# Kernel tuning notes

Measured on AMD Instinct MI355X. Metric: run time of the kernel, lower is better.

Reference implementation:

```python
import jax, jax.numpy as jnp
import numpy as np

NB = 8      # n_blocks
DIM = 256   # model dim (= context_len in source)
DI = 512    # dim_inner = dim * expand(2)
DCONV = 4   # depthwise conv kernel
NS = 16     # d_state
DTR = 16    # dt_rank = ceil(dim/16)
NE = 4      # experts
INNER = 512 # MoE FFN inner = dim * multi(2)
L = 8192    # sequence length
HOR = 32    # horizon
EPS = 1e-3


def setup_inputs() -> dict:
    key = jax.random.key(0)
    ks = jax.random.split(key, 16)
    s = 0.02
    f = lambda k, shp: jax.random.normal(k, shp, jnp.float32) * s
    return {
        "x": jax.random.normal(ks[0], (DIM, L), jnp.float32),
        "lin_w": f(ks[1], (DIM, DIM)),                      # shared by self.linear and self.out (tied)
        "in_proj_w": f(ks[2], (NB, 2 * DI, DIM)),
        "conv_w": f(ks[3], (NB, DI, 1, DCONV)),             # depthwise conv, groups=DI
        "conv_b": f(ks[4], (NB, DI)),
        "x_proj_w": f(ks[5], (NB, DTR + 2 * NS, DI)),
        "dt_proj_w": f(ks[6], (NB, DI, DTR)),
        "dt_proj_b": f(ks[7], (NB, DI)),
        "A_log": jnp.tile(jnp.log(jnp.arange(1, NS + 1, dtype=jnp.float32)), (NB, DI, 1)),
        "D_param": jnp.ones((NB, DI), jnp.float32),
        "out_proj_w": f(ks[8], (NB, DIM, DI)),
        "gate_w": f(ks[9], (NB, NE, DIM)),
        "gproj_w": f(ks[10], (NB, NE, INNER, DIM)),
        "uproj_w": f(ks[11], (NB, NE, INNER, DIM)),
        "dproj_w": f(ks[12], (NB, NE, DIM, INNER)),
        "rms_a_w": jnp.ones((DIM,), jnp.float32),
        "rms_f_w": jnp.ones((DIM,), jnp.float32),
        "head_w1": f(ks[13], (DIM, DIM)),
        "head_w2": f(ks[14], (HOR, DIM)),
    }


def _rmsnorm(h, w):
    return w * (h * jax.lax.rsqrt(jnp.mean(h * h, axis=-1, keepdims=True) + EPS))


def _mamba(h, ipw, cw, cb, xpw, dtw, dtb, alog, dpar, opw):
    b = h.shape[0]
    xr = jnp.einsum('bld,od->bol', h, ipw)            # (b, 2*DI, l)
    xc, res = jnp.split(xr, 2, axis=1)                # each (b, DI, l)
    # causal depthwise conv (padding=DCONV-1, sliced to length l)
    xc = jax.lax.conv_general_dilated(xc, cw, (1,), [(DCONV - 1, 0)],
                                      feature_group_count=DI,
                                      dimension_numbers=('NCH', 'OIH', 'NCH'))
    xc = jax.nn.silu(xc + cb[None, :, None])
    A = -jnp.exp(alog)                                # (DI, NS)
    xdbl = jnp.einsum('bdl,kd->blk', xc, xpw)         # (b, l, DTR+2*NS)
    dr, B, C = xdbl[..., :DTR], xdbl[..., DTR:DTR + NS], xdbl[..., DTR + NS:]
    delta = jax.nn.softplus(jnp.einsum('blr,dr->bld', dr, dtw) + dtb)
    dA = jnp.exp(jnp.einsum('bld,dn->lbdn', delta, A))          # (l, b, DI, NS)
    dBu = jnp.einsum('bld,bln,bdl->lbdn', delta, B, xc)         # (l, b, DI, NS)
    Cl = jnp.transpose(C, (1, 0, 2))                             # (l, b, NS)
    def step(carry, inp):
        a, bu, c = inp
        carry = a * carry + bu
        return carry, jnp.einsum('bdn,bn->bd', carry, c)
    _, ys = jax.lax.scan(step, jnp.zeros((b, DI, NS), xc.dtype), (dA, dBu, Cl))
    y = jnp.transpose(ys, (1, 2, 0)) + xc * dpar[:, None]        # (b, DI, l)
    y = y * jax.nn.silu(res)
    return jnp.einsum('bdl,od->blo', y, opw)                     # (b, l, DIM)


def _moe(h, gw, gp, up, dp):
    shp = h.shape
    xf = h.reshape(-1, shp[-1])                       # (T, DIM)
    scores = xf @ gw.T                                # (T, NE)
    vals, idx = jax.lax.top_k(scores, 2)
    w = jax.nn.softmax(vals, axis=-1)                 # (T, 2)
    g = jax.nn.silu(jnp.einsum('td,ehd->teh', xf, gp))
    u = jnp.einsum('td,ehd->teh', xf, up)
    eo = jnp.einsum('teh,edh->ted', g * u, dp)        # (T, NE, DIM)
    we = jnp.sum(w[..., None] * jax.nn.one_hot(idx, NE, dtype=xf.dtype), axis=1)  # (T, NE)
    return jnp.einsum('te,ted->td', we, eo).reshape(shp)


def reference(x, lin_w, in_proj_w, conv_w, conv_b, x_proj_w, dt_proj_w, dt_proj_b,
              A_log, D_param, out_proj_w, gate_w, gproj_w, uproj_w, dproj_w,
              rms_a_w, rms_f_w, head_w1, head_w2):
    h = x.T[None]                                     # (1, L, DIM)
    h = h @ lin_w.T
    for i in range(NB):
        resi = h
        h = _rmsnorm(h, rms_a_w)
        h = _mamba(h, in_proj_w[i], conv_w[i], conv_b[i], x_proj_w[i],
                   dt_proj_w[i], dt_proj_b[i], A_log[i], D_param[i], out_proj_w[i])
        h = h + resi
        resi = h
        h = _moe(h, gate_w[i], gproj_w[i], uproj_w[i], dproj_w[i])
        h = _rmsnorm(h, rms_f_w)
        h = h + resi
    h = h @ lin_w.T                                   # self.out (tied weight)
    h = jax.nn.silu(h @ head_w1.T) @ head_w2.T        # head
    return jax.nn.sigmoid(h[0].T)                     # (HOR, L)
```

## Files before the change

kernel.cpp:

```cpp
#include <hip/hip_runtime.h>

typedef unsigned short u16;
typedef unsigned int u32;
using bf16x8 = __attribute__((ext_vector_type(8))) short;
using f32x4 = __attribute__((ext_vector_type(4))) float;

constexpr int kL = 8192;
constexpr int kDIM = 256;
constexpr int kDI = 512;
constexpr int kNB = 8;
constexpr float kEPS = 1e-3f;

__device__ __forceinline__ u16 f2b(float f) {
  u32 x = __builtin_bit_cast(u32, f);
  x += 0x7fffu + ((x >> 16) & 1u);
  return (u16)(x >> 16);
}
__device__ __forceinline__ float b2f(u16 u) {
  return __builtin_bit_cast(float, (u32)u << 16);
}
__device__ __forceinline__ float sigm(float x) { return 1.f / (1.f + __expf(-x)); }
__device__ __forceinline__ float softplus_fast(float x) {
  return fmaxf(x, 0.f) + __logf(1.f + __expf(-fabsf(x)));
}

__device__ __forceinline__ void async_cp16(const void* g, void* l) {
  __builtin_amdgcn_global_load_lds((const __attribute__((address_space(1))) u32*)g,
                                   (__attribute__((address_space(3))) u32*)l, 16, 0, 0);
}

struct Cvt2 {
  const float* s[23];
  u16* d[23];
  int n[23];
  int mode[23];
  int bstart[24];
  int nseg;
};
__global__ __launch_bounds__(256) void cvt2_k(Cvt2 dd) {
  const int b = blockIdx.x;
  int seg = 0;
  for (int i = 1; i < dd.nseg; ++i) seg += (b >= dd.bstart[i]) ? 1 : 0;
  const int lb = b - dd.bstart[seg];
  const float* s = dd.s[seg];
  u16* d = dd.d[seg];
  const int n = dd.n[seg];
  const int mode = dd.mode[seg];
  #pragma unroll
  for (int it = 0; it < 4; ++it) {
    const int e4 = lb * 1024 + it * 256 + threadIdx.x;
    const int i = e4 * 4;
    if (i >= n) break;
    const float4 v = ((const float4*)s)[e4];
    ushort4 o = make_ushort4(f2b(v.x), f2b(v.y), f2b(v.z), f2b(v.w));
    size_t dst;
    if (mode == 0) {
      dst = (size_t)i;
    } else if (mode == 1) {
      const int row = i >> 8, col = i & 255;
      const int drow = (row >> 9) * 1024 + ((row >> 4) & 31) * 32 + (row & 15);
      dst = (size_t)drow * 256 + col;
    } else {
      const int bb = i >> 19, e = (i >> 17) & 3, nr = (i >> 9) & 255, j = i & 511;
      dst = (size_t)bb * 524288 + (size_t)nr * 2048 + e * 512 + j;
    }
    *(ushort4*)&d[dst] = o;
  }
}

__global__ __launch_bounds__(256) void transpose_x_k(const float* __restrict__ x, u16* __restrict__ xT) {
  __shared__ float tile[32][33];
  int l0 = blockIdx.x * 32, d0 = blockIdx.y * 32;
  int tx = threadIdx.x, ty = threadIdx.y;
  #pragma unroll
  for (int i = 0; i < 32; i += 8)
    tile[ty + i][tx] = x[(size_t)(d0 + ty + i) * kL + l0 + tx];
  __syncthreads();
  #pragma unroll
  for (int i = 0; i < 32; i += 8)
    xT[(size_t)(l0 + ty + i) * kDIM + d0 + tx] = f2b(tile[tx][ty + i]);
}

template <int BM, int BN, int TR, int TC, int WCN, int MODE>
__global__ __launch_bounds__(256) void gemm_t(
    const u16* __restrict__ A, int lda,
    const u16* __restrict__ W, int ldw,
    void* __restrict__ C, int ldc,
    int N, int K, int pstride)
{
  constexpr int BNR = (BN + 63) & ~63;
  constexpr int NA = BM * 64 / 2048;
  constexpr int NBt = BNR * 64 / 2048;
  __shared__ u16 As[BM * 64];
  __shared__ u16 Bs[BNR * 64];
  const int tid = threadIdx.x;
  const int lane = tid & 63;
  const int wave = tid >> 6;
  const int bm = blockIdx.x * BM;
  const int bn = blockIdx.y * BN;
  const int wrow = (wave / WCN) * (TR * 16);
  const int wcol = (wave % WCN) * (TC * 16);
  const int kchunk = K / (int)gridDim.z;
  const int kbeg = blockIdx.z * kchunk;
  const int niter = kchunk >> 6;

  const u16* aSrc[NA];
  int aDst[NA];
  #pragma unroll
  for (int it = 0; it < NA; ++it) {
    const int flat = (it * 256 + tid) * 8;
    const int r = flat >> 6;
    const int gc = ((((flat >> 3) & 7) ^ (r & 7)) << 3);
    aDst[it] = flat;
    aSrc[it] = A + (size_t)(bm + r) * lda + kbeg + gc;
  }
  const u16* bSrc[NBt];
  int bDst[NBt];
  #pragma unroll
  for (int it = 0; it < NBt; ++it) {
    const int flat = (it * 256 + tid) * 8;
    const int r = flat >> 6;
    const int gc = ((((flat >> 3) & 7) ^ (r & 7)) << 3);
    int n = bn + r;
    if (n > N - 1) n = N - 1;
    bDst[it] = flat;
    bSrc[it] = W + (size_t)n * ldw + kbeg + gc;
  }

  f32x4 acc[TR][TC];
  #pragma unroll
  for (int r = 0; r < TR; ++r)
    #pragma unroll
    for (int c = 0; c < TC; ++c)
      acc[r][c] = f32x4{0.f, 0.f, 0.f, 0.f};

  for (int ki = 0; ki < niter; ++ki) {
    #pragma unroll
    for (int it = 0; it < NA; ++it) {
      async_cp16(aSrc[it], &As[aDst[it]]);
      aSrc[it] += 64;
    }
    #pragma unroll
    for (int it = 0; it < NBt; ++it) {
      async_cp16(bSrc[it], &Bs[bDst[it]]);
      bSrc[it] += 64;
    }
    __syncthreads();
    #pragma unroll
    for (int kk = 0; kk < 64; kk += 32) {
      const int kc = (kk >> 3) + (lane >> 4);
      const int mrow = lane & 15;
      bf16x8 a[TR], b[TC];
      #pragma unroll
      for (int rr = 0; rr < TR; ++rr) {
        int row = wrow + rr * 16 + mrow;
        a[rr] = *(const bf16x8*)&As[row * 64 + ((kc ^ (row & 7)) << 3)];
      }
      #pragma unroll
      for (int cc = 0; cc < TC; ++cc) {
        int row = wcol + cc * 16 + mrow;
        b[cc] = *(const bf16x8*)&Bs[row * 64 + ((kc ^ (row & 7)) << 3)];
      }
      #pragma unroll
      for (int rr = 0; rr < TR; ++rr)
        #pragma unroll
        for (int cc = 0; cc < TC; ++cc)
          acc[rr][cc] = __builtin_amdgcn_mfma_f32_16x16x32_bf16(a[rr], b[cc], acc[rr][cc], 0, 0, 0);
    }
    __syncthreads();
  }

  const int colb = bn + wcol + (lane & 15);
  const int rowb = bm + wrow + ((lane >> 4) << 2);
  #pragma unroll
  for (int rr = 0; rr < TR; ++rr)
    #pragma unroll
    for (int cc = 0; cc < TC; ++cc) {
      int col = colb + cc * 16;
      if (col >= N) continue;
      #pragma unroll
      for (int i = 0; i < 4; ++i) {
        const int row = rowb + rr * 16 + i;
        size_t off = (size_t)row * ldc + col;
        float v = acc[rr][cc][i];
        if constexpr (MODE == 0) ((float*)C)[off] = v;
        else if constexpr (MODE == 2) ((u16*)C)[off] = f2b(v);
        else if constexpr (MODE == 3) ((u16*)C)[off] = f2b(v * sigm(v));
        else if constexpr (MODE == 4) atomicAdd(&((float*)C)[off], v);
        else if constexpr (MODE == 7) ((float*)C)[(size_t)col * kL + row] = sigm(v);
      }
    }
}

__global__ __launch_bounds__(512, 1) void moe_mega_k(
    float* __restrict__ h, const u16* __restrict__ yv, const u16* __restrict__ Wop,
    const float* __restrict__ gw,
    const u16* __restrict__ Wgu, const u16* __restrict__ Wd,
    const float* __restrict__ wf, const float* __restrict__ wa,
    u16* __restrict__ hb2, u16* __restrict__ hn)
{
  __shared__ u16 Ah[32 * 256];
  __shared__ u16 Ts[32 * 512];
  __shared__ u16 Ws[2][256 * 64];
  __shared__ float WeS[32][4];
  const int tid = threadIdx.x;
  const int lane = tid & 63;
  const int quad = lane >> 4;
  const int m16 = lane & 15;
  const int wave = tid >> 6;
  const int wcol = wave * 32;
  const int r0 = blockIdx.x * 32;
  const int prow = tid >> 4;
  const int pcol = (tid & 15) * 16;

  auto stage_op = [&](int buf, int k0) {
    #pragma unroll
    for (int it = 0; it < 4; ++it) {
      const int flat = (it * 512 + tid) * 8;
      const int r = flat >> 6;
      const int gc = ((((flat >> 3) & 7) ^ (r & 7)) << 3);
      async_cp16(Wop + (size_t)r * 512 + k0 + gc, &Ws[buf][flat]);
    }
  };
  auto stage_gu = [&](int buf, int e, int nc, int k0) {
    #pragma unroll
    for (int it = 0; it < 4; ++it) {
      const int flat = (it * 512 + tid) * 8;
      const int r = flat >> 6;
      const int gc = ((((flat >> 3) & 7) ^ (r & 7)) << 3);
      async_cp16(Wgu + (size_t)(e * 1024 + nc * 256 + r) * 256 + k0 + gc, &Ws[buf][flat]);
    }
  };
  auto stage_dp = [&](int buf, int e, int k0) {
    #pragma unroll
    for (int it = 0; it < 4; ++it) {
      const int flat = (it * 512 + tid) * 8;
      const int r = flat >> 6;
      const int gc = ((((flat >> 3) & 7) ^ (r & 7)) << 3);
      async_cp16(Wd + (size_t)r * 2048 + e * 512 + k0 + gc, &Ws[buf][flat]);
    }
  };

  #pragma unroll
  for (int it = 0; it < 4; ++it) {
    const int flat = (it * 512 + tid) * 8;
    const int row = flat >> 9;
    const int c = (flat >> 3) & 63;
    const int cs = (c & ~7) | ((c & 7) ^ (row & 7));
    async_cp16(yv + (size_t)(r0 + row) * 512 + cs * 8, &Ts[flat]);
  }
  f32x4 hacc[2][2];
  #pragma unroll
  for (int rt = 0; rt < 2; ++rt)
    #pragma unroll
    for (int ct = 0; ct < 2; ++ct) hacc[rt][ct] = f32x4{0.f, 0.f, 0.f, 0.f};
  stage_op(0, 0);
  __syncthreads();
  #pragma unroll
  for (int k0i = 0; k0i < 8; ++k0i) {
    if (k0i < 7) stage_op((k0i + 1) & 1, (k0i + 1) * 64);
    const u16* buf = Ws[k0i & 1];
    #pragma unroll
    for (int kk = 0; kk < 64; kk += 32) {
      const int kcs = (kk >> 3) + quad;
      bf16x8 a[2], b[2];
      #pragma unroll
      for (int rt = 0; rt < 2; ++rt) {
        const int row = rt * 16 + m16;
        const int ch = ((k0i * 64 + kk) >> 3) + quad;
        a[rt] = *(const bf16x8*)&Ts[row * 512 + ((ch ^ (row & 7)) << 3)];
      }
      #pragma unroll
      for (int ct = 0; ct < 2; ++ct) {
        const int n = wcol + ct * 16 + m16;
        b[ct] = *(const bf16x8*)&buf[n * 64 + ((kcs ^ (n & 7)) << 3)];
      }
      #pragma unroll
      for (int rt = 0; rt < 2; ++rt)
        #pragma unroll
        for (int ct = 0; ct < 2; ++ct)
          hacc[rt][ct] = __builtin_amdgcn_mfma_f32_16x16x32_bf16(a[rt], b[ct], hacc[rt][ct], 0, 0, 0);
    }
    __syncthreads();
  }
  float* MoeS = (float*)Ts;
  #pragma unroll
  for (int rt = 0; rt < 2; ++rt)
    #pragma unroll
    for (int ct = 0; ct < 2; ++ct)
      #pragma unroll
      for (int i = 0; i < 4; ++i)
        MoeS[(rt * 16 + quad * 4 + i) * 256 + wcol + ct * 16 + m16] = hacc[rt][ct][i];
  __syncthreads();

  float hv[16];
  {
    const size_t base = (size_t)(r0 + prow) * 256 + pcol;
    #pragma unroll
    for (int j = 0; j < 16; j += 4) {
      const float4 v = *(const float4*)(h + base + j);
      hv[j] = v.x + MoeS[prow * 256 + pcol + j];
      hv[j + 1] = v.y + MoeS[prow * 256 + pcol + j + 1];
      hv[j + 2] = v.z + MoeS[prow * 256 + pcol + j + 2];
      hv[j + 3] = v.w + MoeS[prow * 256 + pcol + j + 3];
    }
  }
  {
    float p[4];
    #pragma unroll
    for (int e = 0; e < 4; ++e) {
      float s = 0.f;
      #pragma unroll
      for (int j = 0; j < 16; ++j) s += hv[j] * gw[e * 256 + pcol + j];
      p[e] = s;
    }
    #pragma unroll
    for (int o = 8; o > 0; o >>= 1) {
      p[0] += __shfl_xor(p[0], o); p[1] += __shfl_xor(p[1], o);
      p[2] += __shfl_xor(p[2], o); p[3] += __shfl_xor(p[3], o);
    }
    if ((tid & 15) == 0) {
      int i0 = 0;
      #pragma unroll
      for (int e = 1; e < 4; ++e) if (p[e] > p[i0]) i0 = e;
      int i1 = -1;
      #pragma unroll
      for (int e = 0; e < 4; ++e) {
        if (e == i0) continue;
        if (i1 < 0 || p[e] > p[i1]) i1 = e;
      }
      const float tt = __expf(p[i1] - p[i0]);
      float o0 = 1.f / (1.f + tt), o1 = tt / (1.f + tt);
      WeS[prow][0] = 0.f; WeS[prow][1] = 0.f; WeS[prow][2] = 0.f; WeS[prow][3] = 0.f;
      WeS[prow][i0] = o0; WeS[prow][i1] = o1;
    }
    #pragma unroll
    for (int cc = 0; cc < 2; ++cc) {
      const int chunk = (pcol >> 3) + cc;
      const int sw = ((chunk ^ (prow & 7)) << 3);
      u16 tmp[8];
      #pragma unroll
      for (int j = 0; j < 8; ++j) tmp[j] = f2b(hv[cc * 8 + j]);
      *(bf16x8*)&Ah[prow * 256 + sw] = *(bf16x8*)tmp;
    }
  }
  __syncthreads();

  f32x4 macc[2][2];
  #pragma unroll
  for (int rt = 0; rt < 2; ++rt)
    #pragma unroll
    for (int ct = 0; ct < 2; ++ct) macc[rt][ct] = f32x4{0.f, 0.f, 0.f, 0.f};

  for (int e = 0; e < 4; ++e) {
    for (int nc = 0; nc < 4; ++nc) {
      f32x4 acc[2][2];
      #pragma unroll
      for (int rt = 0; rt < 2; ++rt)
        #pragma unroll
        for (int ct = 0; ct < 2; ++ct) acc[rt][ct] = f32x4{0.f, 0.f, 0.f, 0.f};
      stage_gu(0, e, nc, 0);
      __syncthreads();
      #pragma unroll
      for (int k0i = 0; k0i < 4; ++k0i) {
        if (k0i < 3) stage_gu((k0i + 1) & 1, e, nc, (k0i + 1) * 64);
        const u16* buf = Ws[k0i & 1];
        #pragma unroll
        for (int kk = 0; kk < 64; kk += 32) {
          const int kcs = (kk >> 3) + quad;
          bf16x8 a[2], b[2];
          #pragma unroll
          for (int rt = 0; rt < 2; ++rt) {
            const int row = rt * 16 + m16;
            const int ch = ((k0i * 64 + kk) >> 3) + quad;
            a[rt] = *(const bf16x8*)&Ah[row * 256 + ((ch ^ (row & 7)) << 3)];
          }
          #pragma unroll
          for (int ct = 0; ct < 2; ++ct) {
            const int n = wcol + ct * 16 + m16;
            b[ct] = *(const bf16x8*)&buf[n * 64 + ((kcs ^ (n & 7)) << 3)];
          }
          #pragma unroll
          for (int rt = 0; rt < 2; ++rt)
            #pragma unroll
            for (int ct = 0; ct < 2; ++ct)
              acc[rt][ct] = __builtin_amdgcn_mfma_f32_16x16x32_bf16(a[rt], b[ct], acc[rt][ct], 0, 0, 0);
        }
        __syncthreads();
      }
      const int group = nc * 8 + wave;
      const int j = group * 16 + m16;
      #pragma unroll
      for (int rt = 0; rt < 2; ++rt)
        #pragma unroll
        for (int i = 0; i < 4; ++i) {
          const int row = rt * 16 + quad * 4 + i;
          const float g = acc[rt][0][i];
          const float u = acc[rt][1][i];
          const float val = g * sigm(g) * u * WeS[row][e];
          Ts[row * 512 + (((j >> 3) ^ (row & 7)) << 3) + (j & 7)] = f2b(val);
        }
    }
    __syncthreads();
    stage_dp(0, e, 0);
    __syncthreads();
    #pragma unroll
    for (int k0i = 0; k0i < 8; ++k0i) {
      if (k0i < 7) stage_dp((k0i + 1) & 1, e, (k0i + 1) * 64);
      const u16* buf = Ws[k0i & 1];
      #pragma unroll
      for (int kk = 0; kk < 64; kk += 32) {
        const int kcs = (kk >> 3) + quad;
        bf16x8 a[2], b[2];
        #pragma unroll
        for (int rt = 0; rt < 2; ++rt) {
          const int row = rt * 16 + m16;
          const int ch = ((k0i * 64 + kk) >> 3) + quad;
          a[rt] = *(const bf16x8*)&Ts[row * 512 + ((ch ^ (row & 7)) << 3)];
        }
        #pragma unroll
        for (int ct = 0; ct < 2; ++ct) {
          const int n = wcol + ct * 16 + m16;
          b[ct] = *(const bf16x8*)&buf[n * 64 + ((kcs ^ (n & 7)) << 3)];
        }
        #pragma unroll
        for (int rt = 0; rt < 2; ++rt)
          #pragma unroll
          for (int ct = 0; ct < 2; ++ct)
            macc[rt][ct] = __builtin_amdgcn_mfma_f32_16x16x32_bf16(a[rt], b[ct], macc[rt][ct], 0, 0, 0);
      }
      __syncthreads();
    }
  }

  #pragma unroll
  for (int rt = 0; rt < 2; ++rt)
    #pragma unroll
    for (int ct = 0; ct < 2; ++ct)
      #pragma unroll
      for (int i = 0; i < 4; ++i)
        MoeS[(rt * 16 + quad * 4 + i) * 256 + wcol + ct * 16 + m16] = macc[rt][ct][i];
  __syncthreads();

  float mv[16];
  float ss = 0.f;
  #pragma unroll
  for (int j = 0; j < 16; ++j) {
    mv[j] = MoeS[prow * 256 + pcol + j];
    ss += mv[j] * mv[j];
  }
  #pragma unroll
  for (int o = 8; o > 0; o >>= 1) ss += __shfl_xor(ss, o);
  const float r1 = rsqrtf(ss * (1.f / 256.f) + kEPS);
  float ss2 = 0.f;
  #pragma unroll
  for (int j = 0; j < 16; ++j) {
    hv[j] += wf[pcol + j] * mv[j] * r1;
    ss2 += hv[j] * hv[j];
  }
  #pragma unroll
  for (int o = 8; o > 0; o >>= 1) ss2 += __shfl_xor(ss2, o);
  const float r2 = rsqrtf(ss2 * (1.f / 256.f) + kEPS);

  const size_t base = (size_t)(r0 + prow) * 256 + pcol;
  #pragma unroll
  for (int j = 0; j < 16; j += 4)
    *(float4*)(h + base + j) = float4{hv[j], hv[j + 1], hv[j + 2], hv[j + 3]};
  #pragma unroll
  for (int j = 0; j < 16; j += 4) {
    *(ushort4*)(hb2 + base + j) = make_ushort4(f2b(hv[j]), f2b(hv[j + 1]), f2b(hv[j + 2]), f2b(hv[j + 3]));
    *(ushort4*)(hn + base + j) = make_ushort4(
        f2b(wa[pcol + j] * hv[j] * r2), f2b(wa[pcol + j + 1] * hv[j + 1] * r2),
        f2b(wa[pcol + j + 2] * hv[j + 2] * r2), f2b(wa[pcol + j + 3] * hv[j + 3] * r2));
  }
}

__device__ __forceinline__ float block_sum256(float v) {
  #pragma unroll
  for (int o = 32; o > 0; o >>= 1) v += __shfl_down(v, o);
  __shared__ float red[4];
  __syncthreads();
  if ((threadIdx.x & 63) == 0) red[threadIdx.x >> 6] = v;
  __syncthreads();
  return red[0] + red[1] + red[2] + red[3];
}

__global__ __launch_bounds__(256) void rms_a_k(const float* __restrict__ h, const float* __restrict__ w,
                                               u16* __restrict__ hn) {
  const int l = blockIdx.x, t = threadIdx.x;
  const float v = h[(size_t)l * kDIM + t];
  const float ssum = block_sum256(v * v);
  const float r = rsqrtf(ssum * (1.f / 256.f) + kEPS);
  hn[(size_t)l * kDIM + t] = f2b(w[t] * v * r);
}

__global__ __launch_bounds__(256) void conv_silu_k(const u16* __restrict__ xz, const float* __restrict__ cw,
                                                   const float* __restrict__ cb,
                                                   u16* __restrict__ xcb, u16* __restrict__ zsb,
                                                   float* __restrict__ xdbl) {
  const int i4 = blockIdx.x * 256 + threadIdx.x;
  if (i4 < 98304) *(float4*)&xdbl[i4 * 4] = float4{0.f, 0.f, 0.f, 0.f};
  const int l = i4 >> 7;
  const int d = (i4 & 127) * 4;
  float acc[4];
  const float4 cbv = *(const float4*)&cb[d];
  acc[0] = cbv.x; acc[1] = cbv.y; acc[2] = cbv.z; acc[3] = cbv.w;
  #pragma unroll
  for (int j = 0; j < 4; ++j) {
    const int ll = l - 3 + j;
    if (ll >= 0) {
      const ushort4 xv = *(const ushort4*)&xz[(size_t)ll * 1024 + d];
      acc[0] += cw[(d + 0) * 4 + j] * b2f(xv.x);
      acc[1] += cw[(d + 1) * 4 + j] * b2f(xv.y);
      acc[2] += cw[(d + 2) * 4 + j] * b2f(xv.z);
      acc[3] += cw[(d + 3) * 4 + j] * b2f(xv.w);
    }
  }
  ushort4 xo, zo;
  const ushort4 zv = *(const ushort4*)&xz[(size_t)l * 1024 + 512 + d];
  float z0 = b2f(zv.x), z1 = b2f(zv.y), z2 = b2f(zv.z), z3 = b2f(zv.w);
  xo.x = f2b(acc[0] * sigm(acc[0])); xo.y = f2b(acc[1] * sigm(acc[1]));
  xo.z = f2b(acc[2] * sigm(acc[2])); xo.w = f2b(acc[3] * sigm(acc[3]));
  zo.x = f2b(z0 * sigm(z0)); zo.y = f2b(z1 * sigm(z1));
  zo.z = f2b(z2 * sigm(z2)); zo.w = f2b(z3 * sigm(z3));
  *(ushort4*)&xcb[(size_t)l * 512 + d] = xo;
  *(ushort4*)&zsb[(size_t)l * 512 + d] = zo;
}

__global__ __launch_bounds__(256) void scan_a_k(const float* __restrict__ xdbl, const u16* __restrict__ xcb,
                                                const float* __restrict__ A_log, const float* __restrict__ dtw,
                                                const float* __restrict__ dtb,
                                                u16* __restrict__ delta,
                                                float* __restrict__ aprod, float* __restrict__ bacc) {
  const int c = blockIdx.x;
  const int t = threadIdx.x;
  const int half = t & 1;
  const int d = blockIdx.y * 128 + (t >> 1);
  const int l0 = c * 64;
  __shared__ float Xs[64][32];
  for (int i = t; i < 2048; i += 256)
    Xs[i >> 5][i & 31] = xdbl[(size_t)(l0 + (i >> 5)) * 48 + (i & 31)];
  __syncthreads();
  float wd[8], Ad[8];
  #pragma unroll
  for (int j = 0; j < 8; ++j) wd[j] = dtw[d * 16 + half * 8 + j];
  const float bd = dtb[d];
  #pragma unroll
  for (int n = 0; n < 8; ++n) Ad[n] = -__expf(A_log[d * 16 + half * 8 + n]);
  float s[8], ap[8];
  #pragma unroll
  for (int n = 0; n < 8; ++n) { s[n] = 0.f; ap[n] = 1.f; }
  #pragma unroll 4
  for (int lr = 0; lr < 64; ++lr) {
    const float4 dr0 = *(const float4*)&Xs[lr][half * 8];
    const float4 dr1 = *(const float4*)&Xs[lr][half * 8 + 4];
    float p0 = dr0.x * wd[0] + dr0.y * wd[1] + dr0.z * wd[2] + dr0.w * wd[3];
    float p1 = dr1.x * wd[4] + dr1.y * wd[5] + dr1.z * wd[6] + dr1.w * wd[7];
    float dot = p0 + p1;
    dot += __shfl_xor(dot, 1);
    const float dl = softplus_fast(dot + bd);
    const int l = l0 + lr;
    if (!half) delta[(size_t)l * 512 + d] = f2b(dl);
    const float du = dl * b2f(xcb[(size_t)l * 512 + d]);
    const float4 B0 = *(const float4*)&Xs[lr][16 + half * 8];
    const float4 B1 = *(const float4*)&Xs[lr][16 + half * 8 + 4];
    const float Bv[8] = {B0.x, B0.y, B0.z, B0.w, B1.x, B1.y, B1.z, B1.w};
    #pragma unroll
    for (int n = 0; n < 8; ++n) {
      const float a = __expf(dl * Ad[n]);
      s[n] = fmaf(a, s[n], du * Bv[n]);
      ap[n] *= a;
    }
  }
  const int base = c * 8192 + d * 16 + half * 8;
  #pragma unroll
  for (int n = 0; n < 8; ++n) { aprod[base + n] = ap[n]; bacc[base + n] = s[n]; }
}

__global__ __launch_bounds__(256) void scan_b1_k(const float* __restrict__ aprod, const float* __restrict__ bacc,
                                                 float* __restrict__ gp, float* __restrict__ gb) {
  const int idx = blockIdx.x * 256 + threadIdx.x;
  const int st = idx & 8191, g = idx >> 13;
  float P = 1.f, S = 0.f;
  #pragma unroll
  for (int k = 0; k < 8; ++k) {
    const int c = g * 8 + k;
    const float a = aprod[(size_t)c * 8192 + st];
    S = fmaf(a, S, bacc[(size_t)c * 8192 + st]);
    P *= a;
  }
  gp[(size_t)g * 8192 + st] = P;
  gb[(size_t)g * 8192 + st] = S;
}

__global__ __launch_bounds__(256) void scan_b2_k(const float* __restrict__ gp, const float* __restrict__ gb,
                                                 float* __restrict__ ginit) {
  const int st = blockIdx.x * 256 + threadIdx.x;
  float cur = 0.f;
  #pragma unroll
  for (int g = 0; g < 16; ++g) {
    ginit[(size_t)g * 8192 + st] = cur;
    cur = fmaf(gp[(size_t)g * 8192 + st], cur, gb[(size_t)g * 8192 + st]);
  }
}

__global__ __launch_bounds__(256) void scan_c_k(const float* __restrict__ xdbl, const u16* __restrict__ xcb,
                                                const u16* __restrict__ zsb, const float* __restrict__ A_log,
                                                const u16* __restrict__ delta,
                                                const float* __restrict__ aprod, const float* __restrict__ bacc,
                                                const float* __restrict__ ginit,
                                                const float* __restrict__ Dp, u16* __restrict__ yv) {
  const int c = blockIdx.x;
  const int t = threadIdx.x;
  const int half = t & 1;
  const int d = blockIdx.y * 128 + (t >> 1);
  const int l0 = c * 64;
  __shared__ float Xs[64][32];
  for (int i = t; i < 2048; i += 256)
    Xs[i >> 5][i & 31] = xdbl[(size_t)(l0 + (i >> 5)) * 48 + 16 + (i & 31)];
  __syncthreads();
  float Ad[8];
  #pragma unroll
  for (int n = 0; n < 8; ++n) Ad[n] = -__expf(A_log[d * 16 + half * 8 + n]);
  float s[8];
  {
    const int g = c >> 3;
    const int stb = d * 16 + half * 8;
    const float4 g0 = *(const float4*)&ginit[(size_t)g * 8192 + stb];
    const float4 g1 = *(const float4*)&ginit[(size_t)g * 8192 + stb + 4];
    s[0] = g0.x; s[1] = g0.y; s[2] = g0.z; s[3] = g0.w;
    s[4] = g1.x; s[5] = g1.y; s[6] = g1.z; s[7] = g1.w;
    for (int cc = g * 8; cc < c; ++cc) {
      const float4 a0 = *(const float4*)&aprod[(size_t)cc * 8192 + stb];
      const float4 a1 = *(const float4*)&aprod[(size_t)cc * 8192 + stb + 4];
      const float4 b0 = *(const float4*)&bacc[(size_t)cc * 8192 + stb];
      const float4 b1 = *(const float4*)&bacc[(size_t)cc * 8192 + stb + 4];
      s[0] = fmaf(a0.x, s[0], b0.x); s[1] = fmaf(a0.y, s[1], b0.y);
      s[2] = fmaf(a0.z, s[2], b0.z); s[3] = fmaf(a0.w, s[3], b0.w);
      s[4] = fmaf(a1.x, s[4], b1.x); s[5] = fmaf(a1.y, s[5], b1.y);
      s[6] = fmaf(a1.z, s[6], b1.z); s[7] = fmaf(a1.w, s[7], b1.w);
    }
  }
  const float Dd = Dp[d];
  #pragma unroll 4
  for (int lr = 0; lr < 64; ++lr) {
    const int l = l0 + lr;
    const float dl = b2f(delta[(size_t)l * 512 + d]);
    const float xv = b2f(xcb[(size_t)l * 512 + d]);
    const float zs = b2f(zsb[(size_t)l * 512 + d]);
    const float du = dl * xv;
    const float4 B0 = *(const float4*)&Xs[lr][half * 8];
    const float4 B1 = *(const float4*)&Xs[lr][half * 8 + 4];
    const float4 C0 = *(const float4*)&Xs[lr][16 + half * 8];
    const float4 C1 = *(const float4*)&Xs[lr][16 + half * 8 + 4];
    const float Bv[8] = {B0.x, B0.y, B0.z, B0.w, B1.x, B1.y, B1.z, B1.w};
    const float Cv[8] = {C0.x, C0.y, C0.z, C0.w, C1.x, C1.y, C1.z, C1.w};
    float y = 0.f;
    #pragma unroll
    for (int n = 0; n < 8; ++n) {
      const float a = __expf(dl * Ad[n]);
      s[n] = fmaf(a, s[n], du * Bv[n]);
      y = fmaf(s[n], Cv[n], y);
    }
    y += __shfl_xor(y, 1);
    if (!half) yv[(size_t)l * 512 + d] = f2b((y + xv * Dd) * zs);
  }
}

extern "C" void kernel_launch(void* const* d_in, const int* in_sizes, int n_in,
                              void* d_out, int out_size, void* d_ws, size_t ws_size,
                              hipStream_t stream) {
  const float* x        = (const float*)d_in[0];
  const float* lin_w    = (const float*)d_in[1];
  const float* in_proj  = (const float*)d_in[2];
  const float* conv_w   = (const float*)d_in[3];
  const float* conv_b   = (const float*)d_in[4];
  const float* x_proj   = (const float*)d_in[5];
  const float* dt_w     = (const float*)d_in[6];
  const float* dt_b     = (const float*)d_in[7];
  const float* A_log    = (const float*)d_in[8];
  const float* D_param  = (const float*)d_in[9];
  const float* out_proj = (const float*)d_in[10];
  const float* gate_w   = (const float*)d_in[11];
  const float* gproj    = (const float*)d_in[12];
  const float* uproj    = (const float*)d_in[13];
  const float* dproj    = (const float*)d_in[14];
  const float* rms_a_w  = (const float*)d_in[15];
  const float* rms_f_w  = (const float*)d_in[16];
  const float* head_w1  = (const float*)d_in[17];
  const float* head_w2  = (const float*)d_in[18];

  char* p = (char*)d_ws;
  auto alloc = [&](size_t bytes) -> char* {
    char* r = p;
    p += (bytes + 255) & ~(size_t)255;
    return r;
  };

  u16* lin_b  = (u16*)alloc(65536 * 2);
  u16* ipw_b  = (u16*)alloc((size_t)2097152 * 2);
  u16* xpw_b  = (u16*)alloc((size_t)196608 * 2);
  u16* opw_b  = (u16*)alloc((size_t)1048576 * 2);
  u16* gupw_b = (u16*)alloc((size_t)8388608 * 2);
  u16* dpw_b  = (u16*)alloc((size_t)4194304 * 2);
  u16* hw1_b  = (u16*)alloc(65536 * 2);
  u16* hw2_b  = (u16*)alloc(8192 * 2);

  u16* xT     = (u16*)alloc((size_t)kL * kDIM * 2);
  float* h    = (float*)alloc((size_t)kL * kDIM * 4);
  u16* hn     = (u16*)alloc((size_t)kL * kDIM * 2);
  u16* hb2    = (u16*)alloc((size_t)kL * kDIM * 2);
  float* xdbl = (float*)alloc((size_t)kL * 48 * 4);
  u16* fb     = (u16*)alloc((size_t)kL * kDIM * 2);
  u16* h2b    = (u16*)alloc((size_t)kL * kDIM * 2);
  u16* xz     = (u16*)alloc((size_t)kL * 1024 * 2);
  u16* xcb    = (u16*)alloc((size_t)kL * kDI * 2);
  u16* zsb    = (u16*)alloc((size_t)kL * kDI * 2);
  u16* yv     = (u16*)alloc((size_t)kL * kDI * 2);
  u16* delta  = (u16*)alloc((size_t)kL * kDI * 2);
  float* aprod = (float*)alloc((size_t)128 * 8192 * 4);
  float* bacc  = (float*)alloc((size_t)128 * 8192 * 4);
  float* gp    = (float*)alloc((size_t)16 * 8192 * 4);
  float* gb    = (float*)alloc((size_t)16 * 8192 * 4);
  float* ginit = (float*)alloc((size_t)16 * 8192 * 4);

  if ((size_t)(p - (char*)d_ws) > ws_size) return;

  Cvt2 dd;
  int seg = 0, blk = 0;
  auto add = [&](const float* s, u16* d, int n, int mode) {
    dd.s[seg] = s; dd.d[seg] = d; dd.n[seg] = n; dd.mode[seg] = mode;
    dd.bstart[seg] = blk;
    blk += (n + 4095) / 4096;
    ++seg;
  };
  add(lin_w, lin_b, 65536, 0);
  add(in_proj, ipw_b, 2097152, 0);
  add(x_proj, xpw_b, 196608, 0);
  add(out_proj, opw_b, 1048576, 0);
  add(head_w1, hw1_b, 65536, 0);
  add(head_w2, hw2_b, 8192, 0);
  for (int i = 0; i < kNB; ++i) {
    add(gproj + (size_t)i * 524288, gupw_b + (size_t)i * 1048576, 524288, 1);
    add(uproj + (size_t)i * 524288, gupw_b + (size_t)i * 1048576 + 4096, 524288, 1);
  }
  add(dproj, dpw_b, 4194304, 2);
  dd.nseg = seg;
  dd.bstart[seg] = blk;
  cvt2_k<<<blk, 256, 0, stream>>>(dd);
  transpose_x_k<<<dim3(kL / 32, kDIM / 32), dim3(32, 8), 0, stream>>>(x, xT);

  gemm_t<64, 128, 2, 4, 2, 0><<<dim3(128, 2, 1), 256, 0, stream>>>(
      xT, 256, lin_b, 256, h, 256, 256, 256, 0);
  rms_a_k<<<kL, 256, 0, stream>>>(h, rms_a_w, hn);

  for (int i = 0; i < kNB; ++i) {
    gemm_t<128, 128, 4, 4, 2, 2><<<dim3(64, 8, 1), 256, 0, stream>>>(
        hn, 256, ipw_b + (size_t)i * 262144, 256, xz, 1024, 1024, 256, 0);
    conv_silu_k<<<kL * kDI / 1024, 256, 0, stream>>>(xz, conv_w + (size_t)i * 2048,
                                                     conv_b + (size_t)i * 512, xcb, zsb, xdbl);
    gemm_t<128, 48, 2, 3, 1, 4><<<dim3(64, 1, 8), 256, 0, stream>>>(
        xcb, 512, xpw_b + (size_t)i * 24576, 512, xdbl, 48, 48, 512, 0);
    scan_a_k<<<dim3(128, 4), 256, 0, stream>>>(xdbl, xcb, A_log + (size_t)i * 8192,
                                               dt_w + (size_t)i * 8192, dt_b + (size_t)i * 512,
                                               delta, aprod, bacc);
    scan_b1_k<<<512, 256, 0, stream>>>(aprod, bacc, gp, gb);
    scan_b2_k<<<32, 256, 0, stream>>>(gp, gb, ginit);
    scan_c_k<<<dim3(128, 4), 256, 0, stream>>>(xdbl, xcb, zsb, A_log + (size_t)i * 8192,
                                               delta, aprod, bacc, ginit,
                                               D_param + (size_t)i * 512, yv);
    moe_mega_k<<<256, 512, 0, stream>>>(h, yv, opw_b + (size_t)i * 131072,
                                        gate_w + (size_t)i * 1024,
                                        gupw_b + (size_t)i * 1048576, dpw_b + (size_t)i * 524288,
                                        rms_f_w, rms_a_w, hb2, hn);
  }

  gemm_t<64, 128, 2, 4, 2, 2><<<dim3(128, 2, 1), 256, 0, stream>>>(
      hb2, 256, lin_b, 256, h2b, 256, 256, 256, 0);
  gemm_t<64, 128, 2, 4, 2, 3><<<dim3(128, 2, 1), 256, 0, stream>>>(
      h2b, 256, hw1_b, 256, fb, 256, 256, 256, 0);
  gemm_t<64, 128, 2, 4, 2, 7><<<dim3(128, 1, 1), 256, 0, stream>>>(
      fb, 256, hw2_b, 256, (float*)d_out, 32, 32, 256, 0);
}
```

Before: 1.994 ms.

## Give each wave private weight staging to replace block barriers with wave waits

Weight tiles for the out-proj, gate/up and down-proj GEMMs are now staged per wave. Each wave loads only the 32 weight rows it consumes into its own slice of the double buffer and synchronises with vmcnt waits plus wave barriers instead of block-wide __syncthreads. This removes many block barriers per k-step in the fused post-scan/MoE kernel and lets waves run ahead independently. The trade-off is that each wave issues its own loads with hand-coded waitcnt encodings, which rely on the exact count of outstanding memory operations.

```diff
diff --git a/kernel.cpp b/kernel.cpp
--- a/kernel.cpp
+++ b/kernel.cpp
@@ -28,6 +28,10 @@
   __builtin_amdgcn_global_load_lds((const __attribute__((address_space(1))) u32*)g,
                                    (__attribute__((address_space(3))) u32*)l, 16, 0, 0);
 }
+
+#define WAIT_VM4() __builtin_amdgcn_s_waitcnt(0x0F74)
+#define WAIT_VM0() __builtin_amdgcn_s_waitcnt(0x0F70)
+#define WBAR() __builtin_amdgcn_wave_barrier()
 
 struct Cvt2 {
   const float* s[23];
@@ -213,31 +217,16 @@
   const int prow = tid >> 4;
   const int pcol = (tid & 15) * 16;
 
-  auto stage_op = [&](int buf, int k0) {
+  u16* const myW0 = &Ws[0][wave * 2048];
+  u16* const myW1 = &Ws[1][wave * 2048];
+
+  auto stage_rows = [&](u16* dst, const u16* src, int stride, int k0) {
     #pragma unroll
     for (int it = 0; it < 4; ++it) {
-      const int flat = (it * 512 + tid) * 8;
+      const int flat = (it * 64 + lane) * 8;
       const int r = flat >> 6;
       const int gc = ((((flat >> 3) & 7) ^ (r & 7)) << 3);
-      async_cp16(Wop + (size_t)r * 512 + k0 + gc, &Ws[buf][flat]);
-    }
-  };
-  auto stage_gu = [&](int buf, int e, int nc, int k0) {
-    #pragma unroll
-    for (int it = 0; it < 4; ++it) {
-      const int flat = (it * 512 + tid) * 8;
-      const int r = flat >> 6;
-      const int gc = ((((flat >> 3) & 7) ^ (r & 7)) << 3);
-      async_cp16(Wgu + (size_t)(e * 1024 + nc * 256 + r) * 256 + k0 + gc, &Ws[buf][flat]);
-    }
-  };
-  auto stage_dp = [&](int buf, int e, int k0) {
-    #pragma unroll
-    for (int it = 0; it < 4; ++it) {
-      const int flat = (it * 512 + tid) * 8;
-      const int r = flat >> 6;
-      const int gc = ((((flat >> 3) & 7) ^ (r & 7)) << 3);
-      async_cp16(Wd + (size_t)r * 2048 + e * 512 + k0 + gc, &Ws[buf][flat]);
+      async_cp16(src + (size_t)r * stride + k0 + gc, dst + flat);
     }
   };
 
@@ -249,40 +238,54 @@
     const int cs = (c & ~7) | ((c & 7) ^ (row & 7));
     async_cp16(yv + (size_t)(r0 + row) * 512 + cs * 8, &Ts[flat]);
   }
+  const u16* opsrc = Wop + (size_t)wcol * 512;
+  stage_rows(myW0, opsrc, 512, 0);
+  __syncthreads();
+
   f32x4 hacc[2][2];
   #pragma unroll
   for (int rt = 0; rt < 2; ++rt)
     #pragma unroll
     for (int ct = 0; ct < 2; ++ct) hacc[rt][ct] = f32x4{0.f, 0.f, 0.f, 0.f};
-  stage_op(0, 0);
-  __syncthreads();
-  #pragma unroll
-  for (int k0i = 0; k0i < 8; ++k0i) {
-    if (k0i < 7) stage_op((k0i + 1) & 1, (k0i + 1) * 64);
-    const u16* buf = Ws[k0i & 1];
-    #pragma unroll
-    for (int kk = 0; kk < 64; kk += 32) {
-      const int kcs = (kk >> 3) + quad;
-      bf16x8 a[2], b[2];
-      #pragma unroll
-      for (int rt = 0; rt < 2; ++rt) {
-        const int row = rt * 16 + m16;
-        const int ch = ((k0i * 64 + kk) >> 3) + quad;
-        a[rt] = *(const bf16x8*)&Ts[row * 512 + ((ch ^ (row & 7)) << 3)];
+  {
+    int pb = 0;
+    #pragma unroll
+    for (int k0i = 0; k0i < 8; ++k0i) {
+      if (k0i < 7) {
+        stage_rows(pb ? myW0 : myW1, opsrc, 512, (k0i + 1) * 64);
+        WAIT_VM4();
+      } else {
+        WAIT_VM0();
       }
-      #pragma unroll
-      for (int ct = 0; ct < 2; ++ct) {
-        const int n = wcol + ct * 16 + m16;
-        b[ct] = *(const bf16x8*)&buf[n * 64 + ((kcs ^ (n & 7)) << 3)];
+      WBAR();
+      const u16* buf = pb ? myW1 : myW0;
+      #pragma unroll
+      for (int kk = 0; kk < 64; kk += 32) {
+        const int kcs = (kk >> 3) + quad;
+        bf16x8 a[2], b[2];
+        #pragma unroll
+        for (int rt = 0; rt < 2; ++rt) {
+          const int row = rt * 16 + m16;
+          const int ch = ((k0i * 64 + kk) >> 3) + quad;
+          a[rt] = *(const bf16x8*)&Ts[row * 512 + ((ch ^ (row & 7)) << 3)];
+        }
+        #pragma unroll
+        for (int ct = 0; ct < 2; ++ct) {
+          const int rl = ct * 16 + m16;
+          b[ct] = *(const bf16x8*)&buf[rl * 64 + ((kcs ^ (rl & 7)) << 3)];
+        }
+        #pragma unroll
+        for (int rt = 0; rt < 2; ++rt)
+          #pragma unroll
+          for (int ct = 0; ct < 2; ++ct)
+            hacc[rt][ct] = __builtin_amdgcn_mfma_f32_16x16x32_bf16(a[rt], b[ct], hacc[rt][ct], 0, 0, 0);
       }
-      #pragma unroll
-      for (int rt = 0; rt < 2; ++rt)
-        #pragma unroll
-        for (int ct = 0; ct < 2; ++ct)
-          hacc[rt][ct] = __builtin_amdgcn_mfma_f32_16x16x32_bf16(a[rt], b[ct], hacc[rt][ct], 0, 0, 0);
-    }
-    __syncthreads();
-  }
+      WBAR();
+      pb ^= 1;
+    }
+  }
+  __syncthreads();
+
   float* MoeS = (float*)Ts;
   #pragma unroll
   for (int rt = 0; rt < 2; ++rt)
@@ -353,18 +356,26 @@
     for (int ct = 0; ct < 2; ++ct) macc[rt][ct] = f32x4{0.f, 0.f, 0.f, 0.f};
 
   for (int e = 0; e < 4; ++e) {
+    #pragma unroll
     for (int nc = 0; nc < 4; ++nc) {
       f32x4 acc[2][2];
       #pragma unroll
       for (int rt = 0; rt < 2; ++rt)
         #pragma unroll
         for (int ct = 0; ct < 2; ++ct) acc[rt][ct] = f32x4{0.f, 0.f, 0.f, 0.f};
-      stage_gu(0, e, nc, 0);
-      __syncthreads();
+      const u16* gusrc = Wgu + (size_t)(e * 1024 + nc * 256 + wcol) * 256;
+      stage_rows(myW0, gusrc, 256, 0);
+      int pb = 0;
       #pragma unroll
       for (int k0i = 0; k0i < 4; ++k0i) {
-        if (k0i < 3) stage_gu((k0i + 1) & 1, e, nc, (k0i + 1) * 64);
-        const u16* buf = Ws[k0i & 1];
+        if (k0i < 3) {
+          stage_rows(pb ? myW0 : myW1, gusrc, 256, (k0i + 1) * 64);
+          WAIT_VM4();
+        } else {
+          WAIT_VM0();
+        }
+        WBAR();
+        const u16* buf = pb ? myW1 : myW0;
         #pragma unroll
         for (int kk = 0; kk < 64; kk += 32) {
           const int kcs = (kk >> 3) + quad;
@@ -377,8 +388,8 @@
           }
           #pragma unroll
           for (int ct = 0; ct < 2; ++ct) {
-            const int n = wcol + ct * 16 + m16;
-            b[ct] = *(const bf16x8*)&buf[n * 64 + ((kcs ^ (n & 7)) << 3)];
+            const int rl = ct * 16 + m16;
+            b[ct] = *(const bf16x8*)&buf[rl * 64 + ((kcs ^ (rl & 7)) << 3)];
           }
           #pragma unroll
           for (int rt = 0; rt < 2; ++rt)
@@ -386,7 +397,8 @@
             for (int ct = 0; ct < 2; ++ct)
               acc[rt][ct] = __builtin_amdgcn_mfma_f32_16x16x32_bf16(a[rt], b[ct], acc[rt][ct], 0, 0, 0);
         }
-        __syncthreads();
+        WBAR();
+        pb ^= 1;
       }
       const int group = nc * 8 + wave;
       const int j = group * 16 + m16;
@@ -402,35 +414,46 @@
         }
     }
     __syncthreads();
-    stage_dp(0, e, 0);
+    {
+      const u16* dpsrc = Wd + (size_t)wcol * 2048 + e * 512;
+      stage_rows(myW0, dpsrc, 2048, 0);
+      int pb = 0;
+      #pragma unroll
+      for (int k0i = 0; k0i < 8; ++k0i) {
+        if (k0i < 7) {
+          stage_rows(pb ? myW0 : myW1, dpsrc, 2048, (k0i + 1) * 64);
+          WAIT_VM4();
+        } else {
+          WAIT_VM0();
+        }
+        WBAR();
+        const u16* buf = pb ? myW1 : myW0;
+        #pragma unroll
+        for (int kk = 0; kk < 64; kk += 32) {
+          const int kcs = (kk >> 3) + quad;
+          bf16x8 a[2], b[2];
+          #pragma unroll
+          for (int rt = 0; rt < 2; ++rt) {
+            const int row = rt * 16 + m16;
+            const int ch = ((k0i * 64 + kk) >> 3) + quad;
+            a[rt] = *(const bf16x8*)&Ts[row * 512 + ((ch ^ (row & 7)) << 3)];
+          }
+          #pragma unroll
+          for (int ct = 0; ct < 2; ++ct) {
+            const int rl = ct * 16 + m16;
+            b[ct] = *(const bf16x8*)&buf[rl * 64 + ((kcs ^ (rl & 7)) << 3)];
+          }
+          #pragma unroll
+          for (int rt = 0; rt < 2; ++rt)
+            #pragma unroll
+            for (int ct = 0; ct < 2; ++ct)
+              macc[rt][ct] = __builtin_amdgcn_mfma_f32_16x16x32_bf16(a[rt], b[ct], macc[rt][ct], 0, 0, 0);
+        }
+        WBAR();
+        pb ^= 1;
+      }
+    }
     __syncthreads();
-    #pragma unroll
-    for (int k0i = 0; k0i < 8; ++k0i) {
-      if (k0i < 7) stage_dp((k0i + 1) & 1, e, (k0i + 1) * 64);
-      const u16* buf = Ws[k0i & 1];
-      #pragma unroll
-      for (int kk = 0; kk < 64; kk += 32) {
-        const int kcs = (kk >> 3) + quad;
-        bf16x8 a[2], b[2];
-        #pragma unroll
-        for (int rt = 0; rt < 2; ++rt) {
-          const int row = rt * 16 + m16;
-          const int ch = ((k0i * 64 + kk) >> 3) + quad;
-          a[rt] = *(const bf16x8*)&Ts[row * 512 + ((ch ^ (row & 7)) << 3)];
-        }
-        #pragma unroll
-        for (int ct = 0; ct < 2; ++ct) {
-          const int n = wcol + ct * 16 + m16;
-          b[ct] = *(const bf16x8*)&buf[n * 64 + ((kcs ^ (n & 7)) << 3)];
-        }
-        #pragma unroll
-        for (int rt = 0; rt < 2; ++rt)
-          #pragma unroll
-          for (int ct = 0; ct < 2; ++ct)
-            macc[rt][ct] = __builtin_amdgcn_mfma_f32_16x16x32_bf16(a[rt], b[ct], macc[rt][ct], 0, 0, 0);
-      }
-      __syncthreads();
-    }
   }
 
   #pragma unroll
```

After: 1.753 ms. 12.1% less time.
